# Kernel tuning notes

Hardware: AMD Instinct MI355X
Metric: run time of the kernel (lower is better)

## Reference

```python
import jax, jax.numpy as jnp
import numpy as np

N, E, H, D, L = 50000, 800000, 4, 128, 4
HD = H * D  # 512
NEG_SLOPE_ATTN = 0.2   # DGL GATConv leaky_relu on attention logits
NEG_SLOPE_ACT = 0.01   # F.leaky_relu activation on output
LN_EPS = 1e-5

def _leaky(x, s):
    return jnp.where(x > 0, x, s * x)

def setup_inputs() -> dict:
    key = jax.random.key(0)
    ks = jax.random.split(key, 12)
    features = jax.random.normal(ks[0], (N, D), dtype=jnp.float32)
    src = jax.random.randint(ks[1], (E,), 0, N, dtype=jnp.int32)
    dst = jax.random.randint(ks[2], (E,), 0, N, dtype=jnp.int32)
    s = 0.05
    W_fc   = jax.random.normal(ks[3], (L, D, HD), dtype=jnp.float32) * s
    attn_l = jax.random.normal(ks[4], (L, H, D), dtype=jnp.float32) * s
    attn_r = jax.random.normal(ks[5], (L, H, D), dtype=jnp.float32) * s
    W_res  = jax.random.normal(ks[6], (L, D, HD), dtype=jnp.float32) * s
    b_gat  = jnp.zeros((L, HD), dtype=jnp.float32)
    W_nrm  = jax.random.normal(ks[7], (L, HD, D), dtype=jnp.float32) * s
    b_nrm  = jnp.zeros((L, D), dtype=jnp.float32)
    ln_g   = jnp.ones((L, D), dtype=jnp.float32)
    ln_b   = jnp.zeros((L, D), dtype=jnp.float32)
    return dict(features=features, src=src, dst=dst, W_fc=W_fc, attn_l=attn_l,
                attn_r=attn_r, W_res=W_res, b_gat=b_gat, W_nrm=W_nrm,
                b_nrm=b_nrm, ln_g=ln_g, ln_b=ln_b)

def _gat_layer(x, src, dst, Wf, al, ar, Wr, b):
    feat = (x @ Wf).reshape(N, H, D)                      # [N,H,D]
    el = jnp.einsum('nhd,hd->nh', feat, al)               # [N,H]
    er = jnp.einsum('nhd,hd->nh', feat, ar)
    e = _leaky(el[src] + er[dst], NEG_SLOPE_ATTN)         # [E,H]
    m = jax.ops.segment_max(e, dst, num_segments=N)       # segment softmax over in-edges
    ex = jnp.exp(e - m[dst])
    z = jax.ops.segment_sum(ex, dst, num_segments=N)
    alpha = ex / jnp.maximum(z[dst], 1e-20)               # [E,H]
    msg = feat[src] * alpha[:, :, None]                   # [E,H,D] (dominant traffic)
    rst = jax.ops.segment_sum(msg, dst, num_segments=N)   # [N,H,D]
    rst = rst + (x @ Wr).reshape(N, H, D)                 # linear residual
    rst = rst + b.reshape(H, D)
    rst = _leaky(rst, NEG_SLOPE_ACT)                      # activation
    return rst.reshape(N, HD)

def _layernorm(y, g, b):
    mu = jnp.mean(y, axis=-1, keepdims=True)
    var = jnp.mean(jnp.square(y - mu), axis=-1, keepdims=True)
    return (y - mu) * jax.lax.rsqrt(var + LN_EPS) * g + b

def reference(features, src, dst, W_fc, attn_l, attn_r, W_res, b_gat, W_nrm, b_nrm, ln_g, ln_b):
    x = features
    for l in range(L):
        h = _gat_layer(x, src, dst, W_fc[l], attn_l[l], attn_r[l], W_res[l], b_gat[l])
        y = h @ W_nrm[l] + b_nrm[l]
        x = _layernorm(y, ln_g[l], ln_b[l])
    return x
```

## Files before the change

### kernel.cpp

```cpp
#include <hip/hip_runtime.h>
#include <math.h>

#define NN 50000
#define NPAD 50048
#define EE 800000
#define HH 4
#define DD 128
#define HDIM 512
#define LL 4
#define NB 196

typedef __attribute__((ext_vector_type(8))) short short8;
typedef __attribute__((ext_vector_type(4))) float f32x4;

__device__ __forceinline__ float lk(float x, float s){ return x > 0.f ? x : s*x; }
__device__ __forceinline__ unsigned short f2bf(float f){
  unsigned u = __float_as_uint(f);
  u += 0x7FFFu + ((u >> 16) & 1u);
  return (unsigned short)(u >> 16);
}
__device__ __forceinline__ float lo16(unsigned u){ return __uint_as_float(u << 16); }
__device__ __forceinline__ float hi16(unsigned u){ return __uint_as_float(u & 0xFFFF0000u); }

__global__ void k_zero(int* p, int n){ int i = blockIdx.x*blockDim.x+threadIdx.x; if(i<n) p[i]=0; }

__global__ void k_hist(const int* __restrict__ dst, int* __restrict__ cnt){
  int e = blockIdx.x*blockDim.x+threadIdx.x;
  if (e < EE) atomicAdd(&cnt[dst[e]], 1);
}

__global__ __launch_bounds__(256) void k_bsum(const int* __restrict__ cnt, int* __restrict__ bsum){
  int t = threadIdx.x;
  int i = blockIdx.x*256 + t;
  int v = (i < NN) ? cnt[i] : 0;
  #pragma unroll
  for (int off=32; off>0; off>>=1) v += __shfl_down(v, off);
  __shared__ int ws[4];
  if ((t & 63) == 0) ws[t>>6] = v;
  __syncthreads();
  if (t == 0) bsum[blockIdx.x] = ws[0]+ws[1]+ws[2]+ws[3];
}

__global__ __launch_bounds__(256) void k_bscan(const int* __restrict__ bsum,
                                               int* __restrict__ boff,
                                               int* __restrict__ row_ptr){
  __shared__ int part[256];
  int t = threadIdx.x;
  int v = (t < NB) ? bsum[t] : 0;
  part[t] = v;
  __syncthreads();
  for (int off=1; off<256; off<<=1){
    int u = (t>=off) ? part[t-off] : 0;
    __syncthreads();
    part[t] += u;
    __syncthreads();
  }
  if (t < NB) boff[t] = part[t] - v;
  if (t == 255) row_ptr[NN] = part[255];
}

__global__ __launch_bounds__(256) void k_bfinal(const int* __restrict__ cnt,
                                                const int* __restrict__ boff,
                                                int* __restrict__ row_ptr,
                                                int* __restrict__ cursor){
  __shared__ int part[256];
  int t = threadIdx.x;
  int i = blockIdx.x*256 + t;
  int v = (i < NN) ? cnt[i] : 0;
  part[t] = v;
  __syncthreads();
  for (int off=1; off<256; off<<=1){
    int u = (t>=off) ? part[t-off] : 0;
    __syncthreads();
    part[t] += u;
    __syncthreads();
  }
  if (i < NN){
    int p = boff[blockIdx.x] + part[t] - v;
    row_ptr[i] = p;
    cursor[i]  = p;
  }
}

__global__ void k_fill(const int* __restrict__ src, const int* __restrict__ dst,
                       int* __restrict__ cursor, int* __restrict__ csr_src){
  int e = blockIdx.x*blockDim.x+threadIdx.x;
  if (e >= EE) return;
  int d = dst[e];
  int p = atomicAdd(&cursor[d], 1);
  csr_src[p] = src[e];
}

__global__ __launch_bounds__(256) void k_cvtw2(const float* __restrict__ Wf,
                                               const float* __restrict__ Wr,
                                               unsigned short* __restrict__ W2t){
  __shared__ float tile[64][65];
  int t = threadIdx.x;
  int n0 = blockIdx.x*64, k0 = blockIdx.y*64, l = blockIdx.z;
  const float* srcp = (n0 < 512) ? Wf : Wr;
  int nsrc = (n0 < 512) ? n0 : (n0 - 512);
  #pragma unroll
  for (int j=0;j<16;++j){
    int idx = t + j*256; int kk = idx>>6, nn = idx&63;
    tile[kk][nn] = srcp[(size_t)(l*128 + k0+kk)*512 + nsrc+nn];
  }
  __syncthreads();
  #pragma unroll
  for (int j=0;j<16;++j){
    int idx = t + j*256; int nn = idx>>6, kk = idx&63;
    W2t[((size_t)l*1024 + n0+nn)*128 + k0+kk] = f2bf(tile[kk][nn]);
  }
}
__global__ __launch_bounds__(256) void k_cvtwn(const float* __restrict__ Wn,
                                               unsigned short* __restrict__ Wnt){
  __shared__ float tile[64][65];
  int t = threadIdx.x;
  int n0 = blockIdx.x*64, k0 = blockIdx.y*64, l = blockIdx.z;
  #pragma unroll
  for (int j=0;j<16;++j){
    int idx = t + j*256; int kk = idx>>6, nn = idx&63;
    tile[kk][nn] = Wn[(size_t)(l*512 + k0+kk)*128 + n0+nn];
  }
  __syncthreads();
  #pragma unroll
  for (int j=0;j<16;++j){
    int idx = t + j*256; int nn = idx>>6, kk = idx&63;
    Wnt[((size_t)l*128 + n0+nn)*512 + k0+kk] = f2bf(tile[kk][nn]);
  }
}
__global__ void k_cvtx(const float* __restrict__ x, unsigned short* __restrict__ xb){
  int idx = blockIdx.x*blockDim.x + threadIdx.x;
  int row = idx >> 7;
  xb[idx] = (row < NN) ? f2bf(x[idx]) : (unsigned short)0;
}

__global__ __launch_bounds__(256) void k_gemm1m(const unsigned short* __restrict__ xb,
                                                const unsigned short* __restrict__ W2t,
                                                const float* __restrict__ al,
                                                const float* __restrict__ ar,
                                                unsigned char* __restrict__ featQ,
                                                unsigned short* __restrict__ hbuf,
                                                float2* __restrict__ elsc,
                                                float* __restrict__ erp){
  __shared__ __attribute__((aligned(16))) unsigned short sA[128*136];
  __shared__ __attribute__((aligned(16))) unsigned short sB[128*136];
  __shared__ float sAl[512], sAr[512], sInv[128];
  int t = threadIdx.x;
  int m0 = blockIdx.x*128;
  int isRes = blockIdx.y;
  if (!isRes){
    sAl[t] = al[t]; sAl[256+t] = al[256+t];
    sAr[t] = ar[t]; sAr[256+t] = ar[256+t];
  }
  #pragma unroll
  for (int j=0;j<8;++j){
    int c = t + j*256; int r = c>>4, kc = c&15;
    uint4 v = *(const uint4*)(xb + (size_t)(m0+r)*128 + kc*8);
    *(uint4*)(sA + r*136 + kc*8) = v;
  }
  __syncthreads();

  int lane = t & 63, w = t >> 6;
  int wm = (w & 1)*64, wn = (w >> 1)*64;
  int lrow = lane & 15, quad = lane >> 4;

  short8 af[4][4];
  #pragma unroll
  for (int kq=0;kq<4;++kq){
    int kb = kq*32 + quad*8;
    #pragma unroll
    for (int mt=0;mt<4;++mt) af[kq][mt] = *(const short8*)(sA + (wm+mt*16+lrow)*136 + kb);
  }

  for (int nb=0; nb<4; ++nb){
    int n0 = isRes*512 + nb*128;
    if (nb) __syncthreads();
    #pragma unroll
    for (int j=0;j<8;++j){
      int c = t + j*256; int r = c>>4, kc = c&15;
      uint4 v = *(const uint4*)(W2t + (size_t)(n0+r)*128 + kc*8);
      *(uint4*)(sB + r*136 + kc*8) = v;
    }
    __syncthreads();

    f32x4 acc[4][4];
    #pragma unroll
    for (int mt=0;mt<4;++mt)
      #pragma unroll
      for (int nt=0;nt<4;++nt) acc[mt][nt] = (f32x4){0.f,0.f,0.f,0.f};

    #pragma unroll
    for (int kq=0;kq<4;++kq){
      int kb = kq*32 + quad*8;
      short8 bf[4];
      #pragma unroll
      for (int nt=0;nt<4;++nt) bf[nt] = *(const short8*)(sB + (wn+nt*16+lrow)*136 + kb);
      #pragma unroll
      for (int mt=0;mt<4;++mt)
        #pragma unroll
        for (int nt=0;nt<4;++nt)
          acc[mt][nt] = __builtin_amdgcn_mfma_f32_16x16x32_bf16(af[kq][mt], bf[nt], acc[mt][nt], 0,0,0);
    }

    __syncthreads();
    #pragma unroll
    for (int mt=0;mt<4;++mt)
      #pragma unroll
      for (int nt=0;nt<4;++nt)
        #pragma unroll
        for (int r=0;r<4;++r)
          sB[(wm+mt*16+quad*4+r)*136 + wn+nt*16+lrow] = f2bf(acc[mt][nt][r]);
    __syncthreads();

    if (isRes){
      #pragma unroll
      for (int j=0;j<8;++j){
        int c = t + j*256; int r = c>>4, kc = c&15;
        uint4 v = *(const uint4*)(sB + r*136 + kc*8);
        *(uint4*)(hbuf + (size_t)(m0+r)*512 + nb*128 + kc*8) = v;
      }
    } else {
      int r = t >> 1, half = t & 1;
      int base = half*64;
      float accl = 0.f, accr = 0.f, amax = 0.f;
      #pragma unroll
      for (int d=0; d<64; d+=4){
        uint2 u = *(const uint2*)&sB[r*136 + base + d];
        float f0=lo16(u.x), f1=hi16(u.x), f2=lo16(u.y), f3=hi16(u.y);
        float4 a  = *(const float4*)&sAl[nb*128 + base + d];
        float4 rr = *(const float4*)&sAr[nb*128 + base + d];
        accl += f0*a.x + f1*a.y + f2*a.z + f3*a.w;
        accr += f0*rr.x + f1*rr.y + f2*rr.z + f3*rr.w;
        amax = fmaxf(amax, fmaxf(fmaxf(fabsf(f0), fabsf(f1)), fmaxf(fabsf(f2), fabsf(f3))));
      }
      accl += __shfl_xor(accl, 1);
      accr += __shfl_xor(accr, 1);
      amax = fmaxf(amax, __shfl_xor(amax, 1));
      float am = fmaxf(amax, 1e-8f);
      if (half == 0){
        sInv[r] = 127.f / am;
        if ((m0+r) < NN){
          elsc[(size_t)(m0+r)*4 + nb] = make_float2(accl, am * (1.f/127.f));
          erp[(size_t)(m0+r)*4 + nb] = accr;
        }
      }
      __syncthreads();
      float qinv = sInv[r];
      unsigned char* qdst = featQ + (size_t)(m0+r)*512 + nb*128 + base;
      #pragma unroll
      for (int g=0; g<4; ++g){
        uint4 ua = *(const uint4*)&sB[r*136 + base + g*16];
        uint4 ub = *(const uint4*)&sB[r*136 + base + g*16 + 8];
        unsigned vals[8] = {ua.x, ua.y, ua.z, ua.w, ub.x, ub.y, ub.z, ub.w};
        unsigned p[4];
        #pragma unroll
        for (int j=0;j<4;++j){
          unsigned vlo = vals[2*j], vhi = vals[2*j+1];
          int q0 = (int)rintf(lo16(vlo)*qinv) + 128;
          int q1 = (int)rintf(hi16(vlo)*qinv) + 128;
          int q2 = (int)rintf(lo16(vhi)*qinv) + 128;
          int q3 = (int)rintf(hi16(vhi)*qinv) + 128;
          p[j] = (unsigned)q0 | ((unsigned)q1<<8) | ((unsigned)q2<<16) | ((unsigned)q3<<24);
        }
        *(uint4*)(qdst + g*16) = make_uint4(p[0],p[1],p[2],p[3]);
      }
    }
  }
}

__global__ __launch_bounds__(256) void k_agg(const unsigned char* __restrict__ featQ,
                                             unsigned short* __restrict__ hbuf,
                                             const float2* __restrict__ elsc,
                                             const float* __restrict__ er,
                                             const int* __restrict__ row_ptr,
                                             const int* __restrict__ csr_src,
                                             const float* __restrict__ b_gat){
  int t = threadIdx.x;
  int lane = t & 63;
  int node = blockIdx.x*4 + (t>>6);
  int beg = row_ptr[node], end = row_ptr[node+1];
  int hd = lane >> 4;
  float erh = er[(size_t)node*4 + hd];

  float z = 0.f, sws = 0.f;
  float a0=0.f,a1=0.f,a2=0.f,a3=0.f,a4=0.f,a5=0.f,a6=0.f,a7=0.f;
  const uint2* fQ = (const uint2*)featQ;

  int i = beg;
  for (; i + 3 < end; i += 4){
    int s0 = csr_src[i], s1 = csr_src[i+1], s2 = csr_src[i+2], s3 = csr_src[i+3];
    float2 q0 = elsc[(size_t)s0*4 + hd];
    float2 q1 = elsc[(size_t)s1*4 + hd];
    float2 q2 = elsc[(size_t)s2*4 + hd];
    float2 q3 = elsc[(size_t)s3*4 + hd];
    uint2 f0 = fQ[(size_t)s0*64 + lane];
    uint2 f1 = fQ[(size_t)s1*64 + lane];
    uint2 f2 = fQ[(size_t)s2*64 + lane];
    uint2 f3 = fQ[(size_t)s3*64 + lane];
    float w0 = __expf(lk(q0.x + erh, 0.2f));
    float w1 = __expf(lk(q1.x + erh, 0.2f));
    float w2 = __expf(lk(q2.x + erh, 0.2f));
    float w3 = __expf(lk(q3.x + erh, 0.2f));
    float ws0 = w0*q0.y, ws1 = w1*q1.y, ws2 = w2*q2.y, ws3 = w3*q3.y;
    z += w0 + w1 + w2 + w3;
    sws += ws0 + ws1 + ws2 + ws3;
    a0 += ws0*(float)(f0.x & 255u)      + ws1*(float)(f1.x & 255u)      + ws2*(float)(f2.x & 255u)      + ws3*(float)(f3.x & 255u);
    a1 += ws0*(float)((f0.x>>8) & 255u) + ws1*(float)((f1.x>>8) & 255u) + ws2*(float)((f2.x>>8) & 255u) + ws3*(float)((f3.x>>8) & 255u);
    a2 += ws0*(float)((f0.x>>16)& 255u) + ws1*(float)((f1.x>>16)& 255u) + ws2*(float)((f2.x>>16)& 255u) + ws3*(float)((f3.x>>16)& 255u);
    a3 += ws0*(float)(f0.x>>24)         + ws1*(float)(f1.x>>24)         + ws2*(float)(f2.x>>24)         + ws3*(float)(f3.x>>24);
    a4 += ws0*(float)(f0.y & 255u)      + ws1*(float)(f1.y & 255u)      + ws2*(float)(f2.y & 255u)      + ws3*(float)(f3.y & 255u);
    a5 += ws0*(float)((f0.y>>8) & 255u) + ws1*(float)((f1.y>>8) & 255u) + ws2*(float)((f2.y>>8) & 255u) + ws3*(float)((f3.y>>8) & 255u);
    a6 += ws0*(float)((f0.y>>16)& 255u) + ws1*(float)((f1.y>>16)& 255u) + ws2*(float)((f2.y>>16)& 255u) + ws3*(float)((f3.y>>16)& 255u);
    a7 += ws0*(float)(f0.y>>24)         + ws1*(float)(f1.y>>24)         + ws2*(float)(f2.y>>24)         + ws3*(float)(f3.y>>24);
  }
  for (; i < end; ++i){
    int s = csr_src[i];
    float2 q = elsc[(size_t)s*4 + hd];
    uint2 f = fQ[(size_t)s*64 + lane];
    float w = __expf(lk(q.x + erh, 0.2f));
    float ws = w*q.y;
    z += w; sws += ws;
    a0 += ws*(float)(f.x & 255u);       a1 += ws*(float)((f.x>>8) & 255u);
    a2 += ws*(float)((f.x>>16) & 255u); a3 += ws*(float)(f.x>>24);
    a4 += ws*(float)(f.y & 255u);       a5 += ws*(float)((f.y>>8) & 255u);
    a6 += ws*(float)((f.y>>16) & 255u); a7 += ws*(float)(f.y>>24);
  }
  float iz = 1.f / fmaxf(z, 1e-20f);
  float off = 128.f * sws;

  uint4* rp = (uint4*)(hbuf + (size_t)node*HDIM) + lane;
  uint4 rv = *rp;
  const float4* bp = (const float4*)b_gat;
  float4 b1 = bp[2*lane], b2 = bp[2*lane+1];
  float o0 = lk((a0-off)*iz + lo16(rv.x) + b1.x, 0.01f);
  float o1 = lk((a1-off)*iz + hi16(rv.x) + b1.y, 0.01f);
  float o2 = lk((a2-off)*iz + lo16(rv.y) + b1.z, 0.01f);
  float o3 = lk((a3-off)*iz + hi16(rv.y) + b1.w, 0.01f);
  float o4 = lk((a4-off)*iz + lo16(rv.z) + b2.x, 0.01f);
  float o5 = lk((a5-off)*iz + hi16(rv.z) + b2.y, 0.01f);
  float o6 = lk((a6-off)*iz + lo16(rv.w) + b2.z, 0.01f);
  float o7 = lk((a7-off)*iz + hi16(rv.w) + b2.w, 0.01f);
  uint4 wv;
  wv.x = (unsigned)f2bf(o0) | ((unsigned)f2bf(o1) << 16);
  wv.y = (unsigned)f2bf(o2) | ((unsigned)f2bf(o3) << 16);
  wv.z = (unsigned)f2bf(o4) | ((unsigned)f2bf(o5) << 16);
  wv.w = (unsigned)f2bf(o6) | ((unsigned)f2bf(o7) << 16);
  *rp = wv;
}

__global__ __launch_bounds__(256) void k_gemm3m(const unsigned short* __restrict__ h,
                                                const unsigned short* __restrict__ Wnt,
                                                const float* __restrict__ bn,
                                                const float* __restrict__ lng,
                                                const float* __restrict__ lnb,
                                                float* __restrict__ out,
                                                unsigned short* __restrict__ xb,
                                                int writeOut){
  __shared__ __attribute__((aligned(16))) char smem[2*128*136*2];
  unsigned short* sA = (unsigned short*)smem;
  unsigned short* sB = sA + 128*136;
  float* yf = (float*)smem;
  int t = threadIdx.x;
  int m0 = blockIdx.x*128;
  int lane = t & 63, w = t >> 6;
  int wm = (w & 1)*64, wn = (w >> 1)*64;
  int lrow = lane & 15, quad = lane >> 4;

  f32x4 acc[4][4];
  #pragma unroll
  for (int mt=0;mt<4;++mt)
    #pragma unroll
    for (int nt=0;nt<4;++nt) acc[mt][nt] = (f32x4){0.f,0.f,0.f,0.f};

  for (int kc2=0; kc2<4; ++kc2){
    if (kc2) __syncthreads();
    #pragma unroll
    for (int j=0;j<8;++j){
      int c = t + j*256; int r = c>>4, kc = c&15;
      uint4 v = *(const uint4*)(h + (size_t)(m0+r)*512 + kc2*128 + kc*8);
      *(uint4*)(sA + r*136 + kc*8) = v;
    }
    #pragma unroll
    for (int j=0;j<8;++j){
      int c = t + j*256; int r = c>>4, kc = c&15;
      uint4 v = *(const uint4*)(Wnt + (size_t)r*512 + kc2*128 + kc*8);
      *(uint4*)(sB + r*136 + kc*8) = v;
    }
    __syncthreads();
    #pragma unroll
    for (int kq=0;kq<4;++kq){
      int kb = kq*32 + quad*8;
      short8 af[4], bf[4];
      #pragma unroll
      for (int mt=0;mt<4;++mt) af[mt] = *(const short8*)(sA + (wm+mt*16+lrow)*136 + kb);
      #pragma unroll
      for (int nt=0;nt<4;++nt) bf[nt] = *(const short8*)(sB + (wn+nt*16+lrow)*136 + kb);
      #pragma unroll
      for (int mt=0;mt<4;++mt)
        #pragma unroll
        for (int nt=0;nt<4;++nt)
          acc[mt][nt] = __builtin_amdgcn_mfma_f32_16x16x32_bf16(af[mt], bf[nt], acc[mt][nt], 0,0,0);
    }
  }

  float bnv[4];
  #pragma unroll
  for (int nt=0;nt<4;++nt) bnv[nt] = bn[wn + nt*16 + lrow];
  __syncthreads();
  #pragma unroll
  for (int mt=0;mt<4;++mt)
    #pragma unroll
    for (int nt=0;nt<4;++nt)
      #pragma unroll
      for (int r=0;r<4;++r)
        yf[(wm+mt*16+quad*4+r)*132 + wn+nt*16+lrow] = acc[mt][nt][r] + bnv[nt];
  __syncthreads();

  float g0 = lng[lane], g1 = lng[64+lane];
  float bb0 = lnb[lane], bb1 = lnb[64+lane];
  for (int rr = w*32; rr < w*32+32; ++rr){
    float v0 = yf[rr*132 + lane], v1 = yf[rr*132 + 64 + lane];
    float s = v0 + v1;
    #pragma unroll
    for (int off=32; off>0; off>>=1) s += __shfl_xor(s, off);
    float mu = s * (1.f/128.f);
    float d0 = v0-mu, d1 = v1-mu;
    float q = d0*d0 + d1*d1;
    #pragma unroll
    for (int off=32; off>0; off>>=1) q += __shfl_xor(q, off);
    float inv = rsqrtf(q*(1.f/128.f) + 1e-5f);
    int grow = m0 + rr;
    if (grow < NN){
      float o0 = d0*inv*g0 + bb0;
      float o1 = d1*inv*g1 + bb1;
      xb[(size_t)grow*128 + lane]      = f2bf(o0);
      xb[(size_t)grow*128 + 64 + lane] = f2bf(o1);
      if (writeOut){
        out[(size_t)grow*128 + lane]      = o0;
        out[(size_t)grow*128 + 64 + lane] = o1;
      }
    }
  }
}

extern "C" void kernel_launch(void* const* d_in, const int* in_sizes, int n_in,
                              void* d_out, int out_size, void* d_ws, size_t ws_size,
                              hipStream_t stream){
  const float* features = (const float*)d_in[0];
  const int*   src      = (const int*)d_in[1];
  const int*   dst      = (const int*)d_in[2];
  const float* W_fc     = (const float*)d_in[3];
  const float* attn_l   = (const float*)d_in[4];
  const float* attn_r   = (const float*)d_in[5];
  const float* W_res    = (const float*)d_in[6];
  const float* b_gat    = (const float*)d_in[7];
  const float* W_nrm    = (const float*)d_in[8];
  const float* b_nrm    = (const float*)d_in[9];
  const float* ln_g     = (const float*)d_in[10];
  const float* ln_b     = (const float*)d_in[11];
  float* out = (float*)d_out;

  unsigned short* xb    = (unsigned short*)d_ws;
  unsigned short* hbuf  = xb + (size_t)NPAD*128;
  unsigned short* W2t   = hbuf + (size_t)NPAD*512;
  unsigned short* Wnt   = W2t + (size_t)LL*1024*128;
  unsigned char* featQ  = (unsigned char*)(Wnt + (size_t)LL*128*512);
  float2* elsc = (float2*)(featQ + (size_t)NPAD*512);
  float* er = (float*)(elsc + (size_t)NN*4);
  int* row_ptr = (int*)(er + (size_t)NN*4);
  int* cursor  = row_ptr + (NN+1);
  int* csr_src = cursor + NN;
  int* cnt     = csr_src + EE;
  int* bsum    = cnt + NN;
  int* boff    = bsum + NB;

  k_cvtw2<<<dim3(16, 2, LL), 256, 0, stream>>>(W_fc, W_res, W2t);
  k_cvtwn<<<dim3(2, 8, LL), 256, 0, stream>>>(W_nrm, Wnt);
  k_cvtx<<<(NPAD*128)/256, 256, 0, stream>>>(features, xb);
  k_zero<<<(NN+255)/256, 256, 0, stream>>>(cnt, NN);
  k_hist<<<(EE+255)/256, 256, 0, stream>>>(dst, cnt);
  k_bsum<<<NB, 256, 0, stream>>>(cnt, bsum);
  k_bscan<<<1, 256, 0, stream>>>(bsum, boff, row_ptr);
  k_bfinal<<<NB, 256, 0, stream>>>(cnt, boff, row_ptr, cursor);
  k_fill<<<(EE+255)/256, 256, 0, stream>>>(src, dst, cursor, csr_src);

  for (int l=0; l<LL; ++l){
    const unsigned short* W2l = W2t + (size_t)l*1024*128;
    const unsigned short* Wnl = Wnt + (size_t)l*128*512;
    const float* al = attn_l + (size_t)l*HH*DD;
    const float* ar = attn_r + (size_t)l*HH*DD;
    const float* bg = b_gat  + (size_t)l*HDIM;
    const float* bn = b_nrm  + (size_t)l*DD;
    const float* lg = ln_g   + (size_t)l*DD;
    const float* lb = ln_b   + (size_t)l*DD;

    k_gemm1m<<<dim3(NPAD/128, 2), 256, 0, stream>>>(xb, W2l, al, ar, featQ, hbuf, elsc, er);
    k_agg<<<NN/4, 256, 0, stream>>>(featQ, hbuf, elsc, er, row_ptr, csr_src, bg);
    k_gemm3m<<<NPAD/128, 256, 0, stream>>>(hbuf, Wnl, bn, lg, lb, out, xb, (l==LL-1) ? 1 : 0);
  }
}
```

Before: 784.8 us.

## Fuse norm-projection+LayerNorm with next layer's fc/residual GEMM

Merges the end-of-layer projection and LayerNorm with the next layer's feature/residual GEMM into one kernel, keeping the normalized activations in shared memory instead of writing and rereading them globally. This removes a kernel launch and the xb round trip per layer. In exchange, each block serially computes all eight output column tiles with half the previous grid parallelism, and LayerNorm input is rounded to bf16 before statistics.

```diff
diff --git a/kernel.cpp b/kernel.cpp
--- a/kernel.cpp
+++ b/kernel.cpp
@@ -21,6 +21,7 @@
 }
 __device__ __forceinline__ float lo16(unsigned u){ return __uint_as_float(u << 16); }
 __device__ __forceinline__ float hi16(unsigned u){ return __uint_as_float(u & 0xFFFF0000u); }
+__device__ __forceinline__ float bf2f(unsigned short u){ return __uint_as_float(((unsigned)u) << 16); }
 
 __global__ void k_zero(int* p, int n){ int i = blockIdx.x*blockDim.x+threadIdx.x; if(i<n) p[i]=0; }
 
@@ -132,6 +133,58 @@
   int idx = blockIdx.x*blockDim.x + threadIdx.x;
   int row = idx >> 7;
   xb[idx] = (row < NN) ? f2bf(x[idx]) : (unsigned short)0;
+}
+
+__device__ __forceinline__ void feat_epilogue(const unsigned short* sC, float* sInv,
+                                              const float* sAl, const float* sAr, int hd,
+                                              int m0, int t,
+                                              unsigned char* __restrict__ featQ,
+                                              float2* __restrict__ elsc,
+                                              float* __restrict__ erp){
+  int r = t >> 1, half = t & 1;
+  int base = half*64;
+  float accl = 0.f, accr = 0.f, amax = 0.f;
+  #pragma unroll
+  for (int d=0; d<64; d+=4){
+    uint2 u = *(const uint2*)&sC[r*136 + base + d];
+    float f0=lo16(u.x), f1=hi16(u.x), f2=lo16(u.y), f3=hi16(u.y);
+    float4 a  = *(const float4*)&sAl[hd*128 + base + d];
+    float4 rr = *(const float4*)&sAr[hd*128 + base + d];
+    accl += f0*a.x + f1*a.y + f2*a.z + f3*a.w;
+    accr += f0*rr.x + f1*rr.y + f2*rr.z + f3*rr.w;
+    amax = fmaxf(amax, fmaxf(fmaxf(fabsf(f0), fabsf(f1)), fmaxf(fabsf(f2), fabsf(f3))));
+  }
+  accl += __shfl_xor(accl, 1);
+  accr += __shfl_xor(accr, 1);
+  amax = fmaxf(amax, __shfl_xor(amax, 1));
+  float am = fmaxf(amax, 1e-8f);
+  if (half == 0){
+    sInv[r] = 127.f / am;
+    if ((m0+r) < NN){
+      elsc[(size_t)(m0+r)*4 + hd] = make_float2(accl, am * (1.f/127.f));
+      erp[(size_t)(m0+r)*4 + hd] = accr;
+    }
+  }
+  __syncthreads();
+  float qinv = sInv[r];
+  unsigned char* qdst = featQ + (size_t)(m0+r)*512 + hd*128 + base;
+  #pragma unroll
+  for (int g=0; g<4; ++g){
+    uint4 ua = *(const uint4*)&sC[r*136 + base + g*16];
+    uint4 ub = *(const uint4*)&sC[r*136 + base + g*16 + 8];
+    unsigned vals[8] = {ua.x, ua.y, ua.z, ua.w, ub.x, ub.y, ub.z, ub.w};
+    unsigned p[4];
+    #pragma unroll
+    for (int j=0;j<4;++j){
+      unsigned vlo = vals[2*j], vhi = vals[2*j+1];
+      int q0 = (int)rintf(lo16(vlo)*qinv) + 128;
+      int q1 = (int)rintf(hi16(vlo)*qinv) + 128;
+      int q2 = (int)rintf(lo16(vhi)*qinv) + 128;
+      int q3 = (int)rintf(hi16(vhi)*qinv) + 128;
+      p[j] = (unsigned)q0 | ((unsigned)q1<<8) | ((unsigned)q2<<16) | ((unsigned)q3<<24);
+    }
+    *(uint4*)(qdst + g*16) = make_uint4(p[0],p[1],p[2],p[3]);
+  }
 }
 
 __global__ __launch_bounds__(256) void k_gemm1m(const unsigned short* __restrict__ xb,
@@ -220,50 +273,7 @@
         *(uint4*)(hbuf + (size_t)(m0+r)*512 + nb*128 + kc*8) = v;
       }
     } else {
-      int r = t >> 1, half = t & 1;
-      int base = half*64;
-      float accl = 0.f, accr = 0.f, amax = 0.f;
-      #pragma unroll
-      for (int d=0; d<64; d+=4){
-        uint2 u = *(const uint2*)&sB[r*136 + base + d];
-        float f0=lo16(u.x), f1=hi16(u.x), f2=lo16(u.y), f3=hi16(u.y);
-        float4 a  = *(const float4*)&sAl[nb*128 + base + d];
-        float4 rr = *(const float4*)&sAr[nb*128 + base + d];
-        accl += f0*a.x + f1*a.y + f2*a.z + f3*a.w;
-        accr += f0*rr.x + f1*rr.y + f2*rr.z + f3*rr.w;
-        amax = fmaxf(amax, fmaxf(fmaxf(fabsf(f0), fabsf(f1)), fmaxf(fabsf(f2), fabsf(f3))));
-      }
-      accl += __shfl_xor(accl, 1);
-      accr += __shfl_xor(accr, 1);
-      amax = fmaxf(amax, __shfl_xor(amax, 1));
-      float am = fmaxf(amax, 1e-8f);
-      if (half == 0){
-        sInv[r] = 127.f / am;
-        if ((m0+r) < NN){
-          elsc[(size_t)(m0+r)*4 + nb] = make_float2(accl, am * (1.f/127.f));
-          erp[(size_t)(m0+r)*4 + nb] = accr;
-        }
-      }
-      __syncthreads();
-      float qinv = sInv[r];
-      unsigned char* qdst = featQ + (size_t)(m0+r)*512 + nb*128 + base;
-      #pragma unroll
-      for (int g=0; g<4; ++g){
-        uint4 ua = *(const uint4*)&sB[r*136 + base + g*16];
-        uint4 ub = *(const uint4*)&sB[r*136 + base + g*16 + 8];
-        unsigned vals[8] = {ua.x, ua.y, ua.z, ua.w, ub.x, ub.y, ub.z, ub.w};
-        unsigned p[4];
-        #pragma unroll
-        for (int j=0;j<4;++j){
-          unsigned vlo = vals[2*j], vhi = vals[2*j+1];
-          int q0 = (int)rintf(lo16(vlo)*qinv) + 128;
-          int q1 = (int)rintf(hi16(vlo)*qinv) + 128;
-          int q2 = (int)rintf(lo16(vhi)*qinv) + 128;
-          int q3 = (int)rintf(hi16(vhi)*qinv) + 128;
-          p[j] = (unsigned)q0 | ((unsigned)q1<<8) | ((unsigned)q2<<16) | ((unsigned)q3<<24);
-        }
-        *(uint4*)(qdst + g*16) = make_uint4(p[0],p[1],p[2],p[3]);
-      }
+      feat_epilogue(sB, sInv, sAl, sAr, nb, m0, t, featQ, elsc, erp);
     }
   }
 }
@@ -348,14 +358,162 @@
   *rp = wv;
 }
 
+__global__ __launch_bounds__(256) void k_fused(unsigned short* __restrict__ hbuf,
+                                               const unsigned short* __restrict__ Wnt,
+                                               const float* __restrict__ bn,
+                                               const float* __restrict__ lng,
+                                               const float* __restrict__ lnb,
+                                               const unsigned short* __restrict__ W2t,
+                                               const float* __restrict__ al,
+                                               const float* __restrict__ ar,
+                                               unsigned char* __restrict__ featQ,
+                                               float2* __restrict__ elsc,
+                                               float* __restrict__ erp){
+  __shared__ __attribute__((aligned(16))) unsigned short sA[128*136];
+  __shared__ __attribute__((aligned(16))) unsigned short sB[128*136];
+  __shared__ float sAl[512], sAr[512], sInv[128];
+  int t = threadIdx.x;
+  int m0 = blockIdx.x*128;
+  sAl[t] = al[t]; sAl[256+t] = al[256+t];
+  sAr[t] = ar[t]; sAr[256+t] = ar[256+t];
+  int lane = t & 63, w = t >> 6;
+  int wm = (w & 1)*64, wn = (w >> 1)*64;
+  int lrow = lane & 15, quad = lane >> 4;
+
+  f32x4 acc[4][4];
+  #pragma unroll
+  for (int mt=0;mt<4;++mt)
+    #pragma unroll
+    for (int nt=0;nt<4;++nt) acc[mt][nt] = (f32x4){0.f,0.f,0.f,0.f};
+
+  for (int kc2=0; kc2<4; ++kc2){
+    if (kc2) __syncthreads();
+    #pragma unroll
+    for (int j=0;j<8;++j){
+      int c = t + j*256; int r = c>>4, kc = c&15;
+      uint4 v = *(const uint4*)(hbuf + (size_t)(m0+r)*512 + kc2*128 + kc*8);
+      *(uint4*)(sA + r*136 + kc*8) = v;
+    }
+    #pragma unroll
+    for (int j=0;j<8;++j){
+      int c = t + j*256; int r = c>>4, kc = c&15;
+      uint4 v = *(const uint4*)(Wnt + (size_t)r*512 + kc2*128 + kc*8);
+      *(uint4*)(sB + r*136 + kc*8) = v;
+    }
+    __syncthreads();
+    #pragma unroll
+    for (int kq=0;kq<4;++kq){
+      int kb = kq*32 + quad*8;
+      short8 a4[4], b4[4];
+      #pragma unroll
+      for (int mt=0;mt<4;++mt) a4[mt] = *(const short8*)(sA + (wm+mt*16+lrow)*136 + kb);
+      #pragma unroll
+      for (int nt=0;nt<4;++nt) b4[nt] = *(const short8*)(sB + (wn+nt*16+lrow)*136 + kb);
+      #pragma unroll
+      for (int mt=0;mt<4;++mt)
+        #pragma unroll
+        for (int nt=0;nt<4;++nt)
+          acc[mt][nt] = __builtin_amdgcn_mfma_f32_16x16x32_bf16(a4[mt], b4[nt], acc[mt][nt], 0,0,0);
+    }
+  }
+
+  float bnv[4];
+  #pragma unroll
+  for (int nt=0;nt<4;++nt) bnv[nt] = bn[wn + nt*16 + lrow];
+  __syncthreads();
+  #pragma unroll
+  for (int mt=0;mt<4;++mt)
+    #pragma unroll
+    for (int nt=0;nt<4;++nt)
+      #pragma unroll
+      for (int r=0;r<4;++r)
+        sA[(wm+mt*16+quad*4+r)*136 + wn+nt*16+lrow] = f2bf(acc[mt][nt][r] + bnv[nt]);
+  __syncthreads();
+
+  float g0 = lng[lane], g1 = lng[64+lane];
+  float bb0 = lnb[lane], bb1 = lnb[64+lane];
+  for (int rr = w*32; rr < w*32+32; ++rr){
+    float v0 = bf2f(sA[rr*136 + lane]), v1 = bf2f(sA[rr*136 + 64 + lane]);
+    float s = v0 + v1;
+    #pragma unroll
+    for (int off=32; off>0; off>>=1) s += __shfl_xor(s, off);
+    float mu = s * (1.f/128.f);
+    float d0 = v0-mu, d1 = v1-mu;
+    float q = d0*d0 + d1*d1;
+    #pragma unroll
+    for (int off=32; off>0; off>>=1) q += __shfl_xor(q, off);
+    float inv = rsqrtf(q*(1.f/128.f) + 1e-5f);
+    sA[rr*136 + lane]      = f2bf(d0*inv*g0 + bb0);
+    sA[rr*136 + 64 + lane] = f2bf(d1*inv*g1 + bb1);
+  }
+  __syncthreads();
+
+  short8 af[4][4];
+  #pragma unroll
+  for (int kq=0;kq<4;++kq){
+    int kb = kq*32 + quad*8;
+    #pragma unroll
+    for (int mt=0;mt<4;++mt) af[kq][mt] = *(const short8*)(sA + (wm+mt*16+lrow)*136 + kb);
+  }
+
+  for (int nb=0; nb<8; ++nb){
+    #pragma unroll
+    for (int j=0;j<8;++j){
+      int c = t + j*256; int r = c>>4, kc = c&15;
+      uint4 v = *(const uint4*)(W2t + (size_t)(nb*128+r)*128 + kc*8);
+      *(uint4*)(sB + r*136 + kc*8) = v;
+    }
+    __syncthreads();
+
+    f32x4 ac2[4][4];
+    #pragma unroll
+    for (int mt=0;mt<4;++mt)
+      #pragma unroll
+      for (int nt=0;nt<4;++nt) ac2[mt][nt] = (f32x4){0.f,0.f,0.f,0.f};
+
+    #pragma unroll
+    for (int kq=0;kq<4;++kq){
+      int kb = kq*32 + quad*8;
+      short8 b4[4];
+      #pragma unroll
+      for (int nt=0;nt<4;++nt) b4[nt] = *(const short8*)(sB + (wn+nt*16+lrow)*136 + kb);
+      #pragma unroll
+      for (int mt=0;mt<4;++mt)
+        #pragma unroll
+        for (int nt=0;nt<4;++nt)
+          ac2[mt][nt] = __builtin_amdgcn_mfma_f32_16x16x32_bf16(af[kq][mt], b4[nt], ac2[mt][nt], 0,0,0);
+    }
+
+    __syncthreads();
+    #pragma unroll
+    for (int mt=0;mt<4;++mt)
+      #pragma unroll
+      for (int nt=0;nt<4;++nt)
+        #pragma unroll
+        for (int r=0;r<4;++r)
+          sB[(wm+mt*16+quad*4+r)*136 + wn+nt*16+lrow] = f2bf(ac2[mt][nt][r]);
+    __syncthreads();
+
+    if (nb >= 4){
+      #pragma unroll
+      for (int j=0;j<8;++j){
+        int c = t + j*256; int r = c>>4, kc = c&15;
+        uint4 v = *(const uint4*)(sB + r*136 + kc*8);
+        *(uint4*)(hbuf + (size_t)(m0+r)*512 + (nb-4)*128 + kc*8) = v;
+      }
+    } else {
+      feat_epilogue(sB, sInv, sAl, sAr, nb, m0, t, featQ, elsc, erp);
+    }
+    __syncthreads();
+  }
+}
+
 __global__ __launch_bounds__(256) void k_gemm3m(const unsigned short* __restrict__ h,
                                                 const unsigned short* __restrict__ Wnt,
                                                 const float* __restrict__ bn,
                                                 const float* __restrict__ lng,
                                                 const float* __restrict__ lnb,
-                                                float* __restrict__ out,
-                                                unsigned short* __restrict__ xb,
-                                                int writeOut){
+                                                float* __restrict__ out){
   __shared__ __attribute__((aligned(16))) char smem[2*128*136*2];
   unsigned short* sA = (unsigned short*)smem;
   unsigned short* sB = sA + 128*136;
@@ -390,16 +548,16 @@
     #pragma unroll
     for (int kq=0;kq<4;++kq){
       int kb = kq*32 + quad*8;
-      short8 af[4], bf[4];
-      #pragma unroll
-      for (int mt=0;mt<4;++mt) af[mt] = *(const short8*)(sA + (wm+mt*16+lrow)*136 + kb);
-      #pragma unroll
-      for (int nt=0;nt<4;++nt) bf[nt] = *(const short8*)(sB + (wn+nt*16+lrow)*136 + kb);
+      short8 a4[4], b4[4];
+      #pragma unroll
+      for (int mt=0;mt<4;++mt) a4[mt] = *(const short8*)(sA + (wm+mt*16+lrow)*136 + kb);
+      #pragma unroll
+      for (int nt=0;nt<4;++nt) b4[nt] = *(const short8*)(sB + (wn+nt*16+lrow)*136 + kb);
       #pragma unroll
       for (int mt=0;mt<4;++mt)
         #pragma unroll
         for (int nt=0;nt<4;++nt)
-          acc[mt][nt] = __builtin_amdgcn_mfma_f32_16x16x32_bf16(af[mt], bf[nt], acc[mt][nt], 0,0,0);
+          acc[mt][nt] = __builtin_amdgcn_mfma_f32_16x16x32_bf16(a4[mt], b4[nt], acc[mt][nt], 0,0,0);
     }
   }
 
@@ -431,14 +589,8 @@
     float inv = rsqrtf(q*(1.f/128.f) + 1e-5f);
     int grow = m0 + rr;
     if (grow < NN){
-      float o0 = d0*inv*g0 + bb0;
-      float o1 = d1*inv*g1 + bb1;
-      xb[(size_t)grow*128 + lane]      = f2bf(o0);
-      xb[(size_t)grow*128 + 64 + lane] = f2bf(o1);
-      if (writeOut){
-        out[(size_t)grow*128 + lane]      = o0;
-        out[(size_t)grow*128 + 64 + lane] = o1;
-      }
+      out[(size_t)grow*128 + lane]      = d0*inv*g0 + bb0;
+      out[(size_t)grow*128 + 64 + lane] = d1*inv*g1 + bb1;
     }
   }
 }
@@ -484,18 +636,20 @@
   k_bfinal<<<NB, 256, 0, stream>>>(cnt, boff, row_ptr, cursor);
   k_fill<<<(EE+255)/256, 256, 0, stream>>>(src, dst, cursor, csr_src);
 
-  for (int l=0; l<LL; ++l){
-    const unsigned short* W2l = W2t + (size_t)l*1024*128;
-    const unsigned short* Wnl = Wnt + (size_t)l*128*512;
-    const float* al = attn_l + (size_t)l*HH*DD;
-    const float* ar = attn_r + (size_t)l*HH*DD;
-    const float* bg = b_gat  + (size_t)l*HDIM;
-    const float* bn = b_nrm  + (size_t)l*DD;
-    const float* lg = ln_g   + (size_t)l*DD;
-    const float* lb = ln_b   + (size_t)l*DD;
-
-    k_gemm1m<<<dim3(NPAD/128, 2), 256, 0, stream>>>(xb, W2l, al, ar, featQ, hbuf, elsc, er);
-    k_agg<<<NN/4, 256, 0, stream>>>(featQ, hbuf, elsc, er, row_ptr, csr_src, bg);
-    k_gemm3m<<<NPAD/128, 256, 0, stream>>>(hbuf, Wnl, bn, lg, lb, out, xb, (l==LL-1) ? 1 : 0);
-  }
-}
+  k_gemm1m<<<dim3(NPAD/128, 2), 256, 0, stream>>>(xb, W2t, attn_l, attn_r, featQ, hbuf, elsc, er);
+  k_agg<<<NN/4, 256, 0, stream>>>(featQ, hbuf, elsc, er, row_ptr, csr_src, b_gat);
+
+  for (int l=1; l<LL; ++l){
+    k_fused<<<NPAD/128, 256, 0, stream>>>(hbuf,
+        Wnt + (size_t)(l-1)*128*512, b_nrm + (size_t)(l-1)*DD,
+        ln_g + (size_t)(l-1)*DD, ln_b + (size_t)(l-1)*DD,
+        W2t + (size_t)l*1024*128, attn_l + (size_t)l*HH*DD, attn_r + (size_t)l*HH*DD,
+        featQ, elsc, er);
+    k_agg<<<NN/4, 256, 0, stream>>>(featQ, hbuf, elsc, er, row_ptr, csr_src,
+                                    b_gat + (size_t)l*HDIM);
+  }
+
+  k_gemm3m<<<NPAD/128, 256, 0, stream>>>(hbuf, Wnt + (size_t)3*128*512,
+                                         b_nrm + (size_t)3*DD, ln_g + (size_t)3*DD,
+                                         ln_b + (size_t)3*DD, out);
+}
```

New measurement: 767.6 us. 1.02x faster.
